# Kernel optimization log

Measured on AMD Instinct MI355X. Metric: run time of the kernel, lower is better.

## Reference

```python
import jax, jax.numpy as jnp
import numpy as np

B, IN_DIM, N_NODES, N_LEAVES, N_ACTIONS = 131072, 128, 511, 512, 16


def setup_inputs() -> dict:
    key = jax.random.key(0)
    k1, k2, k3, k4 = jax.random.split(key, 4)
    x = jax.random.normal(k1, (B, IN_DIM), dtype=jnp.float32)
    W1 = jax.random.normal(k2, (N_NODES, IN_DIM), dtype=jnp.float32) * 0.1
    b1 = jax.random.normal(k3, (N_NODES,), dtype=jnp.float32) * 0.1
    W2 = jax.random.normal(k4, (N_LEAVES, 2 * N_NODES), dtype=jnp.float32) * 0.05
    # leaf -> action assignment; arange % n_actions guarantees every group non-empty
    leaf_actions = (jnp.arange(N_LEAVES) % N_ACTIONS).astype(jnp.int32)
    return {"x": x, "W1": W1, "b1": b1, "W2": W2, "leaf_actions": leaf_actions}


def reference(x, W1, b1, W2, leaf_actions):
    # linear1
    h = x @ W1.T + b1                      # [B, N_NODES]
    # relu(h) || relu(-h)
    z = jnp.concatenate([jax.nn.relu(h), jax.nn.relu(-h)], axis=1)  # [B, 2*N_NODES]
    # linear2 (no bias)
    y = z @ W2.T                           # [B, N_LEAVES]
    # grouped segment-max over leaf columns, grouped by action id
    pooled = jax.ops.segment_max(y.T, leaf_actions, num_segments=N_ACTIONS).T  # [B, N_ACTIONS]
    return jax.nn.softmax(pooled, axis=-1)
```

## Files before the change

kernel.cpp:

```cpp
#include <hip/hip_runtime.h>
#include <hip/hip_bf16.h>

typedef unsigned short u16;
typedef unsigned int u32;
typedef __attribute__((ext_vector_type(8))) short bf16x8;
typedef __attribute__((ext_vector_type(4))) float f32x4;

#define NROWS   131072
#define KDIM    128
#define NNODES  511
#define NPAD    512
#define NACT    16

__device__ __forceinline__ u16 f2b(float v) {
  return __builtin_bit_cast(u16, __float2bfloat16(v));
}

union Frag {
  bf16x8 v;
  u16    u[8];
  int4   i;
  int    d[4];
};

__device__ __forceinline__ u32 encf(float f) {
  u32 b = __builtin_bit_cast(u32, f);
  return (b & 0x80000000u) ? ~b : (b | 0x80000000u);
}
__device__ __forceinline__ float decf(u32 u) {
  u32 b = (u & 0x80000000u) ? (u & 0x7FFFFFFFu) : ~u;
  return __builtin_bit_cast(float, b);
}

__global__ void prep_k(const float* __restrict__ W1, const float* __restrict__ W2,
                       const float* __restrict__ b1, u16* __restrict__ w1f,
                       u16* __restrict__ wdf, u16* __restrict__ wsf,
                       float* __restrict__ b1p, u32* __restrict__ outi) {
  int bid = blockIdx.x, t = threadIdx.x;
  if (bid < 256) {
    int o = bid * 256 + t;
    int j = o & 7, l = (o >> 3) & 63, kb = (o >> 9) & 3, nt = o >> 11;
    int row = nt * 16 + (l & 15);
    int col = kb * 32 + (l >> 4) * 8 + j;
    w1f[o] = f2b((row < NNODES) ? W1[row * KDIM + col] : 0.f);
  } else if (bid < 2304) {
    int isS = (bid >= 1280);
    int o = (bid - (isS ? 1280 : 256)) * 256 + t;
    int j = o & 7, l = (o >> 3) & 63, kb = (o >> 9) & 15, lt = o >> 13;
    int leaf = lt * 16 + (l & 15);
    int n = kb * 32 + (l >> 4) * 8 + j;
    float va = 0.f, vb = 0.f;
    if (n < NNODES) {
      va = W2[leaf * (2 * NNODES) + n];
      vb = W2[leaf * (2 * NNODES) + NNODES + n];
    }
    float v = isS ? 0.5f * (va + vb) : 0.5f * (va - vb);
    (isS ? wsf : wdf)[o] = f2b(v);
  } else if (bid < 2306) {
    int i = (bid - 2304) * 256 + t;
    if (i < NPAD) b1p[i] = (i < NNODES) ? b1[i] : 0.f;
  } else {
    int i = (bid - 2306) * 256 + t;
    ((uint4*)outi)[i] = make_uint4(0u, 0u, 0u, 0u);
  }
}

__global__ __launch_bounds__(256, 2) void gemm1_k(const float* __restrict__ x,
                                                  const u16* __restrict__ w1f,
                                                  const float* __restrict__ b1p,
                                                  u16* __restrict__ hb) {
  __shared__ u16 xs[4 * 4 * 64 * 8];
  __shared__ u16 hs[4 * 16 * 64 * 8];

  int t = threadIdx.x, wq = t >> 6, l = t & 63;
  int rg = blockIdx.x;
  int lm = l & 15, quad = l >> 4;

  {
    const float4* xg = (const float4*)(x + (size_t)rg * 64 * KDIM);
#pragma unroll
    for (int i = 0; i < 8; ++i) {
      int f = i * 256 + t;
      int row = f >> 5, col = (f & 31) * 4;
      float4 v = xg[f];
      ushort4 b;
      b.x = f2b(v.x); b.y = f2b(v.y); b.z = f2b(v.z); b.w = f2b(v.w);
      int rt = row >> 4, kb = col >> 5;
      int lane = (row & 15) + 16 * ((col >> 3) & 3);
      *(ushort4*)&xs[(((rt * 4 + kb) * 64 + lane) * 8) + (col & 7)] = b;
    }
  }
  __syncthreads();

  f32x4 zero4 = {0.f, 0.f, 0.f, 0.f};
  f32x4 acc[4][8];
#pragma unroll
  for (int rt = 0; rt < 4; ++rt)
#pragma unroll
    for (int ct = 0; ct < 8; ++ct) acc[rt][ct] = zero4;

#pragma unroll 1
  for (int kb = 0; kb < 4; ++kb) {
    Frag a[4];
#pragma unroll
    for (int rt = 0; rt < 4; ++rt)
      a[rt].i = *(const int4*)&xs[((rt * 4 + kb) * 64 + l) * 8];
#pragma unroll
    for (int ct = 0; ct < 8; ++ct) {
      Frag b;
      b.i = *(const int4*)(w1f + (((wq * 8 + ct) * 4 + kb) * 64 + l) * 8);
#pragma unroll
      for (int rt = 0; rt < 4; ++rt)
        acc[rt][ct] = __builtin_amdgcn_mfma_f32_16x16x32_bf16(a[rt].v, b.v, acc[rt][ct], 0, 0, 0);
    }
  }

#pragma unroll
  for (int ct = 0; ct < 8; ++ct) {
    int node = (wq * 8 + ct) * 16 + lm;
    float bias = b1p[node];
    int kb2 = node >> 5;
    int lsub = 16 * ((node >> 3) & 3);
    int j2 = node & 7;
#pragma unroll
    for (int rt = 0; rt < 4; ++rt)
#pragma unroll
      for (int r = 0; r < 4; ++r) {
        int rl = quad * 4 + r;
        hs[((rt * 16 + kb2) * 64 + (rl + lsub)) * 8 + j2] = f2b(acc[rt][ct][r] + bias);
      }
  }
  __syncthreads();

  {
    int4* dst = (int4*)(hb + (size_t)rg * 32768);
    const int4* src = (const int4*)hs;
#pragma unroll
    for (int i = 0; i < 16; ++i) dst[i * 256 + t] = src[i * 256 + t];
  }
}

__global__ __launch_bounds__(512, 4) void gemm2_k(const u16* __restrict__ hb,
                                                  const u16* __restrict__ wdf,
                                                  const u16* __restrict__ wsf,
                                                  u32* __restrict__ pooled) {
  __shared__ u16 sb[2][40 * 512];

  int t = threadIdx.x, w = t >> 6, l = t & 63;
  int bid = blockIdx.x;
  int half = (bid >> 3) & 1;
  int rg = (bid & 7) | ((bid >> 4) << 3);
  int rh = w >> 2, wq = w & 3;
  int lm = l & 15, quad = l >> 4;

  const u16* gsrc[5];
#pragma unroll
  for (int i = 0; i < 5; ++i) {
    int f = w * 5 + i;
    const u16* p;
    if (f < 8)       p = hb  + ((size_t)(rg * 8 + f) * 16) * 512;
    else if (f < 24) p = wdf + ((size_t)(half * 16 + (f - 8)) * 16) * 512;
    else             p = wsf + ((size_t)(half * 16 + (f - 24)) * 16) * 512;
    gsrc[i] = p + l * 8;
  }

  f32x4 zero4 = {0.f, 0.f, 0.f, 0.f};
  f32x4 acc[4][4];
#pragma unroll
  for (int rt = 0; rt < 4; ++rt)
#pragma unroll
    for (int ct = 0; ct < 4; ++ct) acc[rt][ct] = zero4;

#pragma unroll
  for (int i = 0; i < 5; ++i) {
    int f = w * 5 + i;
    __builtin_amdgcn_global_load_lds(
        (const __attribute__((address_space(1))) void*)(gsrc[i]),
        (__attribute__((address_space(3))) void*)&sb[0][f * 512], 16, 0, 0);
  }
  __syncthreads();

#pragma unroll 1
  for (int kb = 0; kb < 16; ++kb) {
    int cur = kb & 1;
    if (kb < 15) {
#pragma unroll
      for (int i = 0; i < 5; ++i) {
        int f = w * 5 + i;
        __builtin_amdgcn_global_load_lds(
            (const __attribute__((address_space(1))) void*)(gsrc[i] + (kb + 1) * 512),
            (__attribute__((address_space(3))) void*)&sb[cur ^ 1][f * 512], 16, 0, 0);
      }
    }

    Frag h4[4], wA[4], wB[4];
#pragma unroll
    for (int rt = 0; rt < 4; ++rt)
      h4[rt].i = *(const int4*)&sb[cur][(rh * 4 + rt) * 512 + l * 8];
#pragma unroll
    for (int ct = 0; ct < 4; ++ct)
      wA[ct].i = *(const int4*)&sb[cur][(8 + wq * 4 + ct) * 512 + l * 8];
#pragma unroll
    for (int ct = 0; ct < 4; ++ct)
      wB[ct].i = *(const int4*)&sb[cur][(24 + wq * 4 + ct) * 512 + l * 8];

#pragma unroll
    for (int ct = 0; ct < 4; ++ct)
#pragma unroll
      for (int rt = 0; rt < 4; ++rt)
        acc[rt][ct] = __builtin_amdgcn_mfma_f32_16x16x32_bf16(h4[rt].v, wA[ct].v, acc[rt][ct], 0, 0, 0);
#pragma unroll
    for (int rt = 0; rt < 4; ++rt)
#pragma unroll
      for (int d = 0; d < 4; ++d) h4[rt].d[d] &= 0x7FFF7FFF;
#pragma unroll
    for (int ct = 0; ct < 4; ++ct)
#pragma unroll
      for (int rt = 0; rt < 4; ++rt)
        acc[rt][ct] = __builtin_amdgcn_mfma_f32_16x16x32_bf16(h4[rt].v, wB[ct].v, acc[rt][ct], 0, 0, 0);

    __syncthreads();
  }

#pragma unroll
  for (int rt = 0; rt < 4; ++rt)
#pragma unroll
    for (int r = 0; r < 4; ++r) {
      float mx = acc[rt][0][r];
#pragma unroll
      for (int ct = 1; ct < 4; ++ct) mx = fmaxf(mx, acc[rt][ct][r]);
      int row = rg * 128 + rh * 64 + rt * 16 + quad * 4 + r;
      atomicMax(pooled + row * NACT + lm, encf(mx));
    }
}

__global__ void combine_k(u32* __restrict__ outi) {
  int row = blockIdx.x * 256 + threadIdx.x;
  uint4* p = (uint4*)(outi + (size_t)row * NACT);
  uint4 q[4];
#pragma unroll
  for (int i = 0; i < 4; ++i) q[i] = p[i];
  float v[NACT];
#pragma unroll
  for (int i = 0; i < 4; ++i) {
    v[i * 4 + 0] = decf(q[i].x); v[i * 4 + 1] = decf(q[i].y);
    v[i * 4 + 2] = decf(q[i].z); v[i * 4 + 3] = decf(q[i].w);
  }
  float m = v[0];
#pragma unroll
  for (int a = 1; a < NACT; ++a) m = fmaxf(m, v[a]);
  float s = 0.f;
#pragma unroll
  for (int a = 0; a < NACT; ++a) { float e = __expf(v[a] - m); v[a] = e; s += e; }
  float inv = 1.f / s;
  float4* pf = (float4*)(outi + (size_t)row * NACT);
#pragma unroll
  for (int i = 0; i < 4; ++i) {
    float4 o; o.x = v[i*4+0]*inv; o.y = v[i*4+1]*inv; o.z = v[i*4+2]*inv; o.w = v[i*4+3]*inv;
    pf[i] = o;
  }
}

extern "C" void kernel_launch(void* const* d_in, const int* in_sizes, int n_in,
                              void* d_out, int out_size, void* d_ws, size_t ws_size,
                              hipStream_t stream) {
  const float* x  = (const float*)d_in[0];
  const float* W1 = (const float*)d_in[1];
  const float* b1 = (const float*)d_in[2];
  const float* W2 = (const float*)d_in[3];

  char* ws = (char*)d_ws;
  u16*   hb  = (u16*)ws;
  u16*   w1f = (u16*)(ws + 134217728);
  u16*   wdf = (u16*)(ws + 134217728 + 131072);
  u16*   wsf = (u16*)(ws + 134217728 + 131072 + 524288);
  float* b1p = (float*)(ws + 134217728 + 131072 + 524288 + 524288);

  prep_k   <<<dim3(4354), dim3(256), 0, stream>>>(W1, W2, b1, w1f, wdf, wsf, b1p, (u32*)d_out);
  gemm1_k  <<<dim3(NROWS / 64), dim3(256), 0, stream>>>(x, w1f, b1p, hb);
  gemm2_k  <<<dim3(2048), dim3(512), 0, stream>>>(hb, wdf, wsf, (u32*)d_out);
  combine_k<<<dim3(NROWS / 256), dim3(256), 0, stream>>>((u32*)d_out);
}
```

Measured before the change: 266.2 us.

## Fuse softmax into gemm2 via last-block counter and load W_sum fragments directly to registers

The separate combine kernel goes away. Each pair of gemm2 blocks sharing a row group increments a per-group counter, and the second block to arrive reads the atomically max-pooled values and writes the softmax in place. The W_sum operand is no longer staged through LDS: each wave loads its fragments straight from global memory into registers, which shrinks shared memory and may raise occupancy. The cost is a threadfence plus counter atomic per block and extra global load latency inside the k-loop.

```diff
diff --git a/kernel.cpp b/kernel.cpp
--- a/kernel.cpp
+++ b/kernel.cpp
@@ -35,7 +35,8 @@
 __global__ void prep_k(const float* __restrict__ W1, const float* __restrict__ W2,
                        const float* __restrict__ b1, u16* __restrict__ w1f,
                        u16* __restrict__ wdf, u16* __restrict__ wsf,
-                       float* __restrict__ b1p, u32* __restrict__ outi) {
+                       float* __restrict__ b1p, u32* __restrict__ outi,
+                       u32* __restrict__ cnt) {
   int bid = blockIdx.x, t = threadIdx.x;
   if (bid < 256) {
     int o = bid * 256 + t;
@@ -59,9 +60,11 @@
   } else if (bid < 2306) {
     int i = (bid - 2304) * 256 + t;
     if (i < NPAD) b1p[i] = (i < NNODES) ? b1[i] : 0.f;
-  } else {
+  } else if (bid < 4354) {
     int i = (bid - 2306) * 256 + t;
     ((uint4*)outi)[i] = make_uint4(0u, 0u, 0u, 0u);
+  } else {
+    ((uint4*)cnt)[t] = make_uint4(0u, 0u, 0u, 0u);
   }
 }
 
@@ -143,8 +146,10 @@
 __global__ __launch_bounds__(512, 4) void gemm2_k(const u16* __restrict__ hb,
                                                   const u16* __restrict__ wdf,
                                                   const u16* __restrict__ wsf,
-                                                  u32* __restrict__ pooled) {
-  __shared__ u16 sb[2][40 * 512];
+                                                  u32* __restrict__ pooled,
+                                                  u32* __restrict__ cnt) {
+  __shared__ u16 sb[2][24 * 512];
+  __shared__ u32 lastflag;
 
   int t = threadIdx.x, w = t >> 6, l = t & 63;
   int bid = blockIdx.x;
@@ -153,16 +158,16 @@
   int rh = w >> 2, wq = w & 3;
   int lm = l & 15, quad = l >> 4;
 
-  const u16* gsrc[5];
-#pragma unroll
-  for (int i = 0; i < 5; ++i) {
-    int f = w * 5 + i;
+  const u16* gsrc[3];
+#pragma unroll
+  for (int i = 0; i < 3; ++i) {
+    int f = w * 3 + i;
     const u16* p;
-    if (f < 8)       p = hb  + ((size_t)(rg * 8 + f) * 16) * 512;
-    else if (f < 24) p = wdf + ((size_t)(half * 16 + (f - 8)) * 16) * 512;
-    else             p = wsf + ((size_t)(half * 16 + (f - 24)) * 16) * 512;
+    if (f < 8) p = hb  + ((size_t)(rg * 8 + f) * 16) * 512;
+    else       p = wdf + ((size_t)(half * 16 + (f - 8)) * 16) * 512;
     gsrc[i] = p + l * 8;
   }
+  const u16* sbase = wsf + ((size_t)(half * 16 + wq * 4) * 16) * 512 + l * 8;
 
   f32x4 zero4 = {0.f, 0.f, 0.f, 0.f};
   f32x4 acc[4][4];
@@ -172,43 +177,42 @@
     for (int ct = 0; ct < 4; ++ct) acc[rt][ct] = zero4;
 
 #pragma unroll
-  for (int i = 0; i < 5; ++i) {
-    int f = w * 5 + i;
+  for (int i = 0; i < 3; ++i)
     __builtin_amdgcn_global_load_lds(
         (const __attribute__((address_space(1))) void*)(gsrc[i]),
-        (__attribute__((address_space(3))) void*)&sb[0][f * 512], 16, 0, 0);
-  }
+        (__attribute__((address_space(3))) void*)&sb[0][(w * 3 + i) * 512], 16, 0, 0);
   __syncthreads();
 
 #pragma unroll 1
   for (int kb = 0; kb < 16; ++kb) {
     int cur = kb & 1;
+
+    Frag wsr[4];
+#pragma unroll
+    for (int ct = 0; ct < 4; ++ct)
+      wsr[ct].i = *(const int4*)(sbase + ((size_t)(ct * 16 + kb)) * 512);
+
     if (kb < 15) {
 #pragma unroll
-      for (int i = 0; i < 5; ++i) {
-        int f = w * 5 + i;
+      for (int i = 0; i < 3; ++i)
         __builtin_amdgcn_global_load_lds(
             (const __attribute__((address_space(1))) void*)(gsrc[i] + (kb + 1) * 512),
-            (__attribute__((address_space(3))) void*)&sb[cur ^ 1][f * 512], 16, 0, 0);
-      }
-    }
-
-    Frag h4[4], wA[4], wB[4];
+            (__attribute__((address_space(3))) void*)&sb[cur ^ 1][(w * 3 + i) * 512], 16, 0, 0);
+    }
+
+    Frag h4[4], wd4[4];
 #pragma unroll
     for (int rt = 0; rt < 4; ++rt)
       h4[rt].i = *(const int4*)&sb[cur][(rh * 4 + rt) * 512 + l * 8];
 #pragma unroll
     for (int ct = 0; ct < 4; ++ct)
-      wA[ct].i = *(const int4*)&sb[cur][(8 + wq * 4 + ct) * 512 + l * 8];
-#pragma unroll
-    for (int ct = 0; ct < 4; ++ct)
-      wB[ct].i = *(const int4*)&sb[cur][(24 + wq * 4 + ct) * 512 + l * 8];
+      wd4[ct].i = *(const int4*)&sb[cur][(8 + wq * 4 + ct) * 512 + l * 8];
 
 #pragma unroll
     for (int ct = 0; ct < 4; ++ct)
 #pragma unroll
       for (int rt = 0; rt < 4; ++rt)
-        acc[rt][ct] = __builtin_amdgcn_mfma_f32_16x16x32_bf16(h4[rt].v, wA[ct].v, acc[rt][ct], 0, 0, 0);
+        acc[rt][ct] = __builtin_amdgcn_mfma_f32_16x16x32_bf16(h4[rt].v, wd4[ct].v, acc[rt][ct], 0, 0, 0);
 #pragma unroll
     for (int rt = 0; rt < 4; ++rt)
 #pragma unroll
@@ -217,7 +221,7 @@
     for (int ct = 0; ct < 4; ++ct)
 #pragma unroll
       for (int rt = 0; rt < 4; ++rt)
-        acc[rt][ct] = __builtin_amdgcn_mfma_f32_16x16x32_bf16(h4[rt].v, wB[ct].v, acc[rt][ct], 0, 0, 0);
+        acc[rt][ct] = __builtin_amdgcn_mfma_f32_16x16x32_bf16(h4[rt].v, wsr[ct].v, acc[rt][ct], 0, 0, 0);
 
     __syncthreads();
   }
@@ -232,32 +236,36 @@
       int row = rg * 128 + rh * 64 + rt * 16 + quad * 4 + r;
       atomicMax(pooled + row * NACT + lm, encf(mx));
     }
-}
-
-__global__ void combine_k(u32* __restrict__ outi) {
-  int row = blockIdx.x * 256 + threadIdx.x;
-  uint4* p = (uint4*)(outi + (size_t)row * NACT);
-  uint4 q[4];
-#pragma unroll
-  for (int i = 0; i < 4; ++i) q[i] = p[i];
-  float v[NACT];
-#pragma unroll
-  for (int i = 0; i < 4; ++i) {
-    v[i * 4 + 0] = decf(q[i].x); v[i * 4 + 1] = decf(q[i].y);
-    v[i * 4 + 2] = decf(q[i].z); v[i * 4 + 3] = decf(q[i].w);
-  }
-  float m = v[0];
-#pragma unroll
-  for (int a = 1; a < NACT; ++a) m = fmaxf(m, v[a]);
-  float s = 0.f;
-#pragma unroll
-  for (int a = 0; a < NACT; ++a) { float e = __expf(v[a] - m); v[a] = e; s += e; }
-  float inv = 1.f / s;
-  float4* pf = (float4*)(outi + (size_t)row * NACT);
-#pragma unroll
-  for (int i = 0; i < 4; ++i) {
-    float4 o; o.x = v[i*4+0]*inv; o.y = v[i*4+1]*inv; o.z = v[i*4+2]*inv; o.w = v[i*4+3]*inv;
-    pf[i] = o;
+
+  __threadfence();
+  __syncthreads();
+  if (t == 0) lastflag = atomicAdd(&cnt[rg], 1u);
+  __syncthreads();
+  if (lastflag == 1u && t < 128) {
+    __threadfence();
+    int row = rg * 128 + t;
+    float v[NACT];
+#pragma unroll
+    for (int a = 0; a < NACT; ++a) {
+      u32 q = __hip_atomic_load(&pooled[(size_t)row * NACT + a],
+                                __ATOMIC_RELAXED, __HIP_MEMORY_SCOPE_AGENT);
+      v[a] = decf(q);
+    }
+    float m = v[0];
+#pragma unroll
+    for (int a = 1; a < NACT; ++a) m = fmaxf(m, v[a]);
+    float s = 0.f;
+#pragma unroll
+    for (int a = 0; a < NACT; ++a) { float e = __expf(v[a] - m); v[a] = e; s += e; }
+    float inv = 1.f / s;
+    float4* pf = (float4*)(pooled + (size_t)row * NACT);
+#pragma unroll
+    for (int i = 0; i < 4; ++i) {
+      float4 o;
+      o.x = v[i * 4 + 0] * inv; o.y = v[i * 4 + 1] * inv;
+      o.z = v[i * 4 + 2] * inv; o.w = v[i * 4 + 3] * inv;
+      pf[i] = o;
+    }
   }
 }
 
@@ -272,12 +280,13 @@
   char* ws = (char*)d_ws;
   u16*   hb  = (u16*)ws;
   u16*   w1f = (u16*)(ws + 134217728);
-  u16*   wdf = (u16*)(ws + 134217728 + 131072);
-  u16*   wsf = (u16*)(ws + 134217728 + 131072 + 524288);
-  float* b1p = (float*)(ws + 134217728 + 131072 + 524288 + 524288);
-
-  prep_k   <<<dim3(4354), dim3(256), 0, stream>>>(W1, W2, b1, w1f, wdf, wsf, b1p, (u32*)d_out);
-  gemm1_k  <<<dim3(NROWS / 64), dim3(256), 0, stream>>>(x, w1f, b1p, hb);
-  gemm2_k  <<<dim3(2048), dim3(512), 0, stream>>>(hb, wdf, wsf, (u32*)d_out);
-  combine_k<<<dim3(NROWS / 256), dim3(256), 0, stream>>>((u32*)d_out);
-}
+  u16*   wdf = (u16*)(ws + 134348800);
+  u16*   wsf = (u16*)(ws + 134873088);
+  float* b1p = (float*)(ws + 135397376);
+  u32*   cnt = (u32*)(ws + 135399424);
+
+  prep_k  <<<dim3(4355), dim3(256), 0, stream>>>(W1, W2, b1, w1f, wdf, wsf, b1p,
+                                                 (u32*)d_out, cnt);
+  gemm1_k <<<dim3(NROWS / 64), dim3(256), 0, stream>>>(x, w1f, b1p, hb);
+  gemm2_k <<<dim3(2048), dim3(512), 0, stream>>>(hb, wdf, wsf, (u32*)d_out, cnt);
+}
```

Measured after the change: 708.8 us. 166% more time.
